# Optimization experiments

Hardware: AMD Instinct MI355X
Metric: run time of the kernel (lower is better)

The kernel has to match this reference:

```python
import jax, jax.numpy as jnp
import numpy as np

B, LAT, MEM, IMG = 8192, 256, 200, 128
THRESHOLD = 1.0 / MEM          # sparse-addressing threshold 1/MEM_DIM
EPS_SHRINK = 1e-12             # module epsilon
EPS_COS = 1e-8                 # torch CosineSimilarity default eps
EPS_L1 = 1e-12                 # torch F.normalize default eps


def setup_inputs() -> dict:
    key = jax.random.key(0)
    k1, k2, k3 = jax.random.split(key, 3)
    z = jax.random.normal(k1, (B, LAT), dtype=jnp.float32)          # encoder latent
    memory = jax.random.normal(k2, (MEM, LAT), dtype=jnp.float32) * 0.05  # kaiming-scale memory
    W = jax.random.normal(k3, (IMG * IMG, LAT), dtype=jnp.float32) * 0.02  # linear weight
    b = jnp.zeros((IMG * IMG,), dtype=jnp.float32)
    return {"z": z, "memory": memory, "W": W, "b": b}


def reference(z, memory, W, b):
    # Cosine similarity via normalized matmul (no [B,MEM,LAT] repeat tensors)
    zn = jnp.linalg.norm(z, axis=1, keepdims=True)          # [B,1]
    mn = jnp.linalg.norm(memory, axis=1, keepdims=True)     # [MEM,1]
    logits = (z @ memory.T) / jnp.maximum(zn * mn.T, EPS_COS)  # [B,MEM]
    w = jax.nn.softmax(logits, axis=1)
    # sparse shrinkage: relu(w-t)*w/(|w-t|+eps)
    w = jax.nn.relu(w - THRESHOLD) * w / (jnp.abs(w - THRESHOLD) + EPS_SHRINK)
    # L1 normalize over memory dim
    w = w / jnp.maximum(jnp.sum(jnp.abs(w), axis=1, keepdims=True), EPS_L1)
    z_hat = w @ memory                                      # [B,LAT]
    x_hat = (z_hat @ W.T + b).reshape(-1, 1, IMG, IMG)      # [B,1,128,128]
    return x_hat, z_hat, w
```

## Files before the change

### kernel.cpp

```cpp
#include <hip/hip_runtime.h>
#include <hip/hip_bf16.h>
#include <stdint.h>

#define B_DIM   8192
#define LAT     256
#define MEM_DIM 200
#define MEM_PAD 208
#define NPIX    16384
#define RPB     16
#define CHUNK   25

typedef short bf16x8 __attribute__((ext_vector_type(8)));
typedef float f32x4  __attribute__((ext_vector_type(4)));

__device__ __forceinline__ float wred_sum(float v) {
#pragma unroll
  for (int m = 32; m; m >>= 1) v += __shfl_xor(v, m, 64);
  return v;
}
__device__ __forceinline__ float wred_max(float v) {
#pragma unroll
  for (int m = 32; m; m >>= 1) v = fmaxf(v, __shfl_xor(v, m, 64));
  return v;
}
__device__ __forceinline__ unsigned short f2bf(float f) {
  unsigned u = __builtin_bit_cast(unsigned, f);
  u = u + 0x7FFFu + ((u >> 16) & 1u);
  return (unsigned short)(u >> 16);
}
__device__ __forceinline__ float bf2f(unsigned short h) {
  return __builtin_bit_cast(float, (unsigned)h << 16);
}
__device__ __forceinline__ void split3(float v, unsigned short& h, unsigned short& m,
                                       unsigned short& l) {
  h = f2bf(v);
  float r1 = v - bf2f(h);
  m = f2bf(r1);
  float r2 = r1 - bf2f(m);
  l = f2bf(r2);
}

__global__ void __launch_bounds__(64) mem_norm_kernel(const float* __restrict__ mem,
                                                      float* __restrict__ mn,
                                                      unsigned short* __restrict__ mem_h,
                                                      unsigned short* __restrict__ mem_m,
                                                      unsigned short* __restrict__ mem_l) {
  const int m = blockIdx.x, lane = threadIdx.x;
  if (m >= MEM_DIM) {
    ushort4 zz = {0, 0, 0, 0};
    ((ushort4*)(mem_h + (size_t)m * LAT))[lane] = zz;
    ((ushort4*)(mem_m + (size_t)m * LAT))[lane] = zz;
    ((ushort4*)(mem_l + (size_t)m * LAT))[lane] = zz;
    return;
  }
  float4 v = ((const float4*)(mem + (size_t)m * LAT))[lane];
  ushort4 h, md, l;
  split3(v.x, h.x, md.x, l.x); split3(v.y, h.y, md.y, l.y);
  split3(v.z, h.z, md.z, l.z); split3(v.w, h.w, md.w, l.w);
  ((ushort4*)(mem_h + (size_t)m * LAT))[lane] = h;
  ((ushort4*)(mem_m + (size_t)m * LAT))[lane] = md;
  ((ushort4*)(mem_l + (size_t)m * LAT))[lane] = l;
  float ss = v.x * v.x + v.y * v.y + v.z * v.z + v.w * v.w;
  ss = wred_sum(ss);
  if (lane == 0) mn[m] = sqrtf(ss);
}

__global__ void __launch_bounds__(256) zsplit_kernel(const float* __restrict__ z,
                                                     unsigned short* __restrict__ z_h,
                                                     unsigned short* __restrict__ z_m,
                                                     unsigned short* __restrict__ z_l) {
  const int i = blockIdx.x * 256 + threadIdx.x;
  float4 v = ((const float4*)z)[i];
  ushort4 h, md, l;
  split3(v.x, h.x, md.x, l.x); split3(v.y, h.y, md.y, l.y);
  split3(v.z, h.z, md.z, l.z); split3(v.w, h.w, md.w, l.w);
  ((ushort4*)z_h)[i] = h;
  ((ushort4*)z_m)[i] = md;
  ((ushort4*)z_l)[i] = l;
}

__global__ void __launch_bounds__(256) convert_w_kernel(const float* __restrict__ W,
                                                        unsigned short* __restrict__ Wb) {
  const int i = blockIdx.x * 256 + threadIdx.x;
  float4 v = ((const float4*)W)[i];
  ushort4 o;
  o.x = f2bf(v.x); o.y = f2bf(v.y); o.z = f2bf(v.z); o.w = f2bf(v.w);
  ((ushort4*)Wb)[i] = o;
}

__global__ void __launch_bounds__(256) row_kernel(
    const float* __restrict__ z, const float* __restrict__ mem,
    const float* __restrict__ mn_g,
    const unsigned short* __restrict__ z_h, const unsigned short* __restrict__ z_m,
    const unsigned short* __restrict__ z_l,
    const unsigned short* __restrict__ mem_h, const unsigned short* __restrict__ mem_m,
    const unsigned short* __restrict__ mem_l,
    float* __restrict__ zhat_out, float* __restrict__ w_out,
    unsigned short* __restrict__ zhat_bf) {
  __shared__ float msh[CHUNK * LAT];
  __shared__ float lw[RPB][MEM_DIM];
  __shared__ float mnsh[MEM_DIM];

  const int tid = threadIdx.x;
  const int lane = tid & 63;
  const int wid = tid >> 6;
  const int row0 = blockIdx.x * RPB;

  if (tid < MEM_DIM) mnsh[tid] = mn_g[tid];

  float4 zr[4];
  float zn[4];
#pragma unroll
  for (int r = 0; r < 4; ++r) {
    const int row = row0 + wid * 4 + r;
    zr[r] = *(const float4*)(z + (size_t)row * LAT + lane * 4);
    float ss = zr[r].x * zr[r].x + zr[r].y * zr[r].y + zr[r].z * zr[r].z + zr[r].w * zr[r].w;
    zn[r] = sqrtf(wred_sum(ss));
  }

  {
    const int fr_ = lane & 15;
    const int kq8 = (lane >> 4) * 8;
    const size_t zoff = (size_t)(row0 + fr_) * LAT + kq8;
    const unsigned short* zh_p = z_h + zoff;
    const unsigned short* zm_p = z_m + zoff;
    const unsigned short* zl_p = z_l + zoff;
    for (int nf = wid; nf <= 12; nf += 4) {
      const size_t moff = (size_t)(nf * 16 + fr_) * LAT + kq8;
      const unsigned short* mh_p = mem_h + moff;
      const unsigned short* mm_p = mem_m + moff;
      const unsigned short* ml_p = mem_l + moff;
      f32x4 a = {};
#pragma unroll
      for (int kk = 0; kk < 8; ++kk) {
        bf16x8 zh = *(const bf16x8*)(zh_p + kk * 32);
        bf16x8 zm = *(const bf16x8*)(zm_p + kk * 32);
        bf16x8 zl = *(const bf16x8*)(zl_p + kk * 32);
        bf16x8 mh = *(const bf16x8*)(mh_p + kk * 32);
        bf16x8 mm = *(const bf16x8*)(mm_p + kk * 32);
        bf16x8 ml = *(const bf16x8*)(ml_p + kk * 32);
        a = __builtin_amdgcn_mfma_f32_16x16x32_bf16(zm, mm, a, 0, 0, 0);
        a = __builtin_amdgcn_mfma_f32_16x16x32_bf16(zh, ml, a, 0, 0, 0);
        a = __builtin_amdgcn_mfma_f32_16x16x32_bf16(zl, mh, a, 0, 0, 0);
        a = __builtin_amdgcn_mfma_f32_16x16x32_bf16(zm, mh, a, 0, 0, 0);
        a = __builtin_amdgcn_mfma_f32_16x16x32_bf16(zh, mm, a, 0, 0, 0);
        a = __builtin_amdgcn_mfma_f32_16x16x32_bf16(zh, mh, a, 0, 0, 0);
      }
      const int m = nf * 16 + fr_;
      if (m < MEM_DIM) {
#pragma unroll
        for (int q = 0; q < 4; ++q)
          lw[(lane >> 4) * 4 + q][m] = a[q];
      }
    }
  }
  __syncthreads();

  const float t = 0.005f;
#pragma unroll
  for (int r = 0; r < 4; ++r) {
    const int lr = wid * 4 + r;
    float lg[4];
#pragma unroll
    for (int i = 0; i < 4; ++i) {
      const int m = lane + 64 * i;
      lg[i] = (m < MEM_DIM) ? lw[lr][m] / fmaxf(zn[r] * mnsh[m], 1e-8f) : -1e30f;
    }
    float mx = wred_max(fmaxf(fmaxf(lg[0], lg[1]), fmaxf(lg[2], lg[3])));
    float e[4]; float s = 0.f;
#pragma unroll
    for (int i = 0; i < 4; ++i) {
      const int m = lane + 64 * i;
      e[i] = (m < MEM_DIM) ? expf(lg[i] - mx) : 0.f;
      s += e[i];
    }
    s = wred_sum(s);
    float sv[4]; float l1 = 0.f;
#pragma unroll
    for (int i = 0; i < 4; ++i) {
      const float wv = e[i] / s;
      const float d = wv - t;
      sv[i] = fmaxf(d, 0.f) * wv / (fabsf(d) + 1e-12f);
      l1 += sv[i];
    }
    l1 = wred_sum(l1);
    const float dnm = fmaxf(l1, 1e-12f);
#pragma unroll
    for (int i = 0; i < 4; ++i) {
      const int m = lane + 64 * i;
      if (m < MEM_DIM) {
        const float wn = sv[i] / dnm;
        lw[lr][m] = wn;
        w_out[(size_t)(row0 + lr) * MEM_DIM + m] = wn;
      }
    }
  }

  f32x4 acc[4] = {};
  for (int c = 0; c < 8; ++c) {
    __syncthreads();
    const float4* gsrc = (const float4*)(mem + (size_t)c * CHUNK * LAT);
    float4* msh4 = (float4*)msh;
    for (int i = tid; i < CHUNK * 64; i += 256) msh4[i] = gsrc[i];
    __syncthreads();
    for (int mm = 0; mm < CHUNK; ++mm) {
      float4 mv = ((float4*)msh)[mm * 64 + lane];
      const int m = c * CHUNK + mm;
#pragma unroll
      for (int r = 0; r < 4; ++r) {
        const float wm = lw[wid * 4 + r][m];
        acc[r][0] += wm * mv.x; acc[r][1] += wm * mv.y;
        acc[r][2] += wm * mv.z; acc[r][3] += wm * mv.w;
      }
    }
  }
#pragma unroll
  for (int r = 0; r < 4; ++r) {
    const int row = row0 + wid * 4 + r;
    float4 o; o.x = acc[r][0]; o.y = acc[r][1]; o.z = acc[r][2]; o.w = acc[r][3];
    *(float4*)(zhat_out + (size_t)row * LAT + lane * 4) = o;
    ushort4 ob; ob.x = f2bf(o.x); ob.y = f2bf(o.y); ob.z = f2bf(o.z); ob.w = f2bf(o.w);
    *(ushort4*)(zhat_bf + (size_t)row * LAT + lane * 4) = ob;
  }
}

#define TSTRIDE 68
__global__ void __launch_bounds__(256, 3) gemm_xhat_kernel(
    const unsigned short* __restrict__ A,
    const unsigned short* __restrict__ Bw,
    const float* __restrict__ bias,
    float* __restrict__ C) {
  __shared__ __align__(16) unsigned char smem[49152];

  const int tid = threadIdx.x;
  const int lane = tid & 63;
  const int wid = tid >> 6;

  const int swz = (blockIdx.x & 7) * 1024 + (blockIdx.x >> 3);
  const int st = swz >> 8;
  const int loc = swz & 255;
  const int tm = (st >> 3) * 16 + (loc & 15);
  const int tn = (st & 7) * 16 + (loc >> 4);
  const int brow = tm * 128;
  const int bcol = tn * 128;

  const int wr = wid >> 1, wc = wid & 1;

  const int ch0 = wid * 2;
  const int r0 = ch0 * 16 + (lane >> 2);
  const int kq = (lane & 3) * 8;

  f32x4 acc[4][4] = {};

#define STAGE(bufbase, t)                                                      \
  {                                                                            \
    const int k0_ = (t) * 32;                                                  \
    _Pragma("unroll")                                                          \
    for (int cc = 0; cc < 2; ++cc) {                                           \
      const int r_ = r0 + cc * 16;                                             \
      __builtin_amdgcn_global_load_lds(                                        \
          (const __attribute__((address_space(1))) void*)(const void*)         \
              (A + (size_t)(brow + r_) * LAT + k0_ + kq),                      \
          (__attribute__((address_space(3))) void*)(void*)                     \
              &smem[(bufbase) + (ch0 + cc) * 1024], 16, 0, 0);                 \
      __builtin_amdgcn_global_load_lds(                                        \
          (const __attribute__((address_space(1))) void*)(const void*)         \
              (Bw + (size_t)(bcol + r_) * LAT + k0_ + kq),                     \
          (__attribute__((address_space(3))) void*)(void*)                     \
              &smem[(bufbase) + 8192 + (ch0 + cc) * 1024], 16, 0, 0);          \
    }                                                                          \
  }

  STAGE(0, 0);
  STAGE(16384, 1);
  STAGE(32768, 2);

#pragma unroll
  for (int t = 0; t < 8; ++t) {
    if (t < 6)       asm volatile("s_waitcnt vmcnt(8)" ::: "memory");
    else if (t == 6) asm volatile("s_waitcnt vmcnt(4)" ::: "memory");
    else             asm volatile("s_waitcnt vmcnt(0)" ::: "memory");
    __builtin_amdgcn_sched_barrier(0);
    __builtin_amdgcn_s_barrier();

    const int bufb = (t % 3) * 16384;
    bf16x8 af[4], bfr[4];
#pragma unroll
    for (int mf = 0; mf < 4; ++mf)
      af[mf] = *(const bf16x8*)&smem[bufb + (wr * 64 + mf * 16 + (lane & 15)) * 64 + (lane >> 4) * 16];
#pragma unroll
    for (int nf = 0; nf < 4; ++nf)
      bfr[nf] = *(const bf16x8*)&smem[bufb + 8192 + (wc * 64 + nf * 16 + (lane & 15)) * 64 + (lane >> 4) * 16];

    asm volatile("s_waitcnt lgkmcnt(0)" ::: "memory");
    __builtin_amdgcn_sched_barrier(0);
    __builtin_amdgcn_s_barrier();

    if (t + 3 < 8) STAGE(((t + 3) % 3) * 16384, t + 3);

#pragma unroll
    for (int mf = 0; mf < 4; ++mf)
#pragma unroll
      for (int nf = 0; nf < 4; ++nf)
        acc[mf][nf] = __builtin_amdgcn_mfma_f32_16x16x32_bf16(af[mf], bfr[nf], acc[mf][nf], 0, 0, 0);
  }
#undef STAGE

  __syncthreads();
  float* tt = (float*)(smem + wid * (16 * TSTRIDE * 4));

  const int colq = (lane & 15) * 4;
  const int col0 = bcol + wc * 64 + colq;
  const float4 bv4 = *(const float4*)(bias + col0);

#pragma unroll
  for (int mf = 0; mf < 4; ++mf) {
#pragma unroll
    for (int nf = 0; nf < 4; ++nf) {
      const int cl = nf * 16 + (lane & 15);
#pragma unroll
      for (int q = 0; q < 4; ++q)
        tt[((lane >> 4) * 4 + q) * TSTRIDE + cl] = acc[mf][nf][q];
    }
#pragma unroll
    for (int rr = 0; rr < 4; ++rr) {
      const int rl = rr * 4 + (lane >> 4);
      float4 v = *(const float4*)&tt[rl * TSTRIDE + colq];
      v.x += bv4.x; v.y += bv4.y; v.z += bv4.z; v.w += bv4.w;
      const int row = brow + wr * 64 + mf * 16 + rl;
      *(float4*)&C[(size_t)row * NPIX + col0] = v;
    }
  }
}

extern "C" void kernel_launch(void* const* d_in, const int* in_sizes, int n_in,
                              void* d_out, int out_size, void* d_ws, size_t ws_size,
                              hipStream_t stream) {
  const float* z    = (const float*)d_in[0];
  const float* mem  = (const float*)d_in[1];
  const float* W    = (const float*)d_in[2];
  const float* bias = (const float*)d_in[3];

  float* xhat = (float*)d_out;
  float* zhat = xhat + (size_t)B_DIM * NPIX;
  float* wout = zhat + (size_t)B_DIM * LAT;

  unsigned short* z_h   = (unsigned short*)xhat;
  unsigned short* z_m   = z_h + (size_t)B_DIM * LAT;
  unsigned short* z_l   = z_m + (size_t)B_DIM * LAT;
  unsigned short* mem_h = z_l + (size_t)B_DIM * LAT;
  unsigned short* mem_m = mem_h + (size_t)MEM_PAD * LAT;
  unsigned short* mem_l = mem_m + (size_t)MEM_PAD * LAT;

  unsigned short* Wb  = (unsigned short*)d_ws;
  unsigned short* zhb = Wb + (size_t)NPIX * LAT;
  float* mn = (float*)(zhb + (size_t)B_DIM * LAT);

  mem_norm_kernel<<<MEM_PAD, 64, 0, stream>>>(mem, mn, mem_h, mem_m, mem_l);
  zsplit_kernel<<<(B_DIM * LAT / 4) / 256, 256, 0, stream>>>(z, z_h, z_m, z_l);
  convert_w_kernel<<<(NPIX * LAT / 4) / 256, 256, 0, stream>>>(W, Wb);
  row_kernel<<<B_DIM / RPB, 256, 0, stream>>>(z, mem, mn, z_h, z_m, z_l,
                                              mem_h, mem_m, mem_l, zhat, wout, zhb);
  gemm_xhat_kernel<<<8192, 256, 0, stream>>>(zhb, Wb, bias, xhat);
}
```

Measured before the change: 223.4 us.

## Use double-buffered pipeline and direct MFMA-transposed epilogue in xhat GEMM

Replaces the triple-buffered global_load_lds pipeline with explicit vmcnt waits by a simpler double buffer synchronized with __syncthreads, cutting LDS use to 32KB and raising launch bounds to 4 blocks per CU. It swaps the MFMA operand order so each lane's accumulator holds 4 consecutive columns. That lets the epilogue write float4 directly to C instead of transposing through LDS. The cost is less prefetch depth and a full barrier each iteration, traded for higher occupancy and no LDS round trip in the output store.

```diff
diff --git a/kernel.cpp b/kernel.cpp
--- a/kernel.cpp
+++ b/kernel.cpp
@@ -224,13 +224,10 @@
   }
 }
 
-#define TSTRIDE 68
-__global__ void __launch_bounds__(256, 3) gemm_xhat_kernel(
-    const unsigned short* __restrict__ A,
-    const unsigned short* __restrict__ Bw,
-    const float* __restrict__ bias,
-    float* __restrict__ C) {
-  __shared__ __align__(16) unsigned char smem[49152];
+__global__ void __launch_bounds__(256, 4) gemm_xhat_kernel(
+    const unsigned short* __restrict__ A, const unsigned short* __restrict__ Bw,
+    const float* __restrict__ bias, float* __restrict__ C) {
+  __shared__ __align__(16) unsigned char smem[32768];
 
   const int tid = threadIdx.x;
   const int lane = tid & 63;
@@ -272,18 +269,13 @@
   }
 
   STAGE(0, 0);
-  STAGE(16384, 1);
-  STAGE(32768, 2);
+  __syncthreads();
 
 #pragma unroll
   for (int t = 0; t < 8; ++t) {
-    if (t < 6)       asm volatile("s_waitcnt vmcnt(8)" ::: "memory");
-    else if (t == 6) asm volatile("s_waitcnt vmcnt(4)" ::: "memory");
-    else             asm volatile("s_waitcnt vmcnt(0)" ::: "memory");
-    __builtin_amdgcn_sched_barrier(0);
-    __builtin_amdgcn_s_barrier();
-
-    const int bufb = (t % 3) * 16384;
+    const int bufb = (t & 1) * 16384;
+    if (t < 7) STAGE(bufb ^ 16384, t + 1);
+
     bf16x8 af[4], bfr[4];
 #pragma unroll
     for (int mf = 0; mf < 4; ++mf)
@@ -292,43 +284,31 @@
     for (int nf = 0; nf < 4; ++nf)
       bfr[nf] = *(const bf16x8*)&smem[bufb + 8192 + (wc * 64 + nf * 16 + (lane & 15)) * 64 + (lane >> 4) * 16];
 
-    asm volatile("s_waitcnt lgkmcnt(0)" ::: "memory");
-    __builtin_amdgcn_sched_barrier(0);
-    __builtin_amdgcn_s_barrier();
-
-    if (t + 3 < 8) STAGE(((t + 3) % 3) * 16384, t + 3);
-
 #pragma unroll
     for (int mf = 0; mf < 4; ++mf)
 #pragma unroll
       for (int nf = 0; nf < 4; ++nf)
-        acc[mf][nf] = __builtin_amdgcn_mfma_f32_16x16x32_bf16(af[mf], bfr[nf], acc[mf][nf], 0, 0, 0);
+        acc[mf][nf] = __builtin_amdgcn_mfma_f32_16x16x32_bf16(bfr[nf], af[mf], acc[mf][nf], 0, 0, 0);
+
+    if (t < 7) __syncthreads();
   }
 #undef STAGE
 
-  __syncthreads();
-  float* tt = (float*)(smem + wid * (16 * TSTRIDE * 4));
-
-  const int colq = (lane & 15) * 4;
-  const int col0 = bcol + wc * 64 + colq;
-  const float4 bv4 = *(const float4*)(bias + col0);
+  const int crow0 = brow + wr * 64 + (lane & 15);
+  const int ccol0 = bcol + wc * 64 + (lane >> 4) * 4;
+  float4 bv[4];
+#pragma unroll
+  for (int nf = 0; nf < 4; ++nf)
+    bv[nf] = *(const float4*)(bias + ccol0 + nf * 16);
 
 #pragma unroll
   for (int mf = 0; mf < 4; ++mf) {
+    float* crow_p = C + (size_t)(crow0 + mf * 16) * NPIX;
 #pragma unroll
     for (int nf = 0; nf < 4; ++nf) {
-      const int cl = nf * 16 + (lane & 15);
-#pragma unroll
-      for (int q = 0; q < 4; ++q)
-        tt[((lane >> 4) * 4 + q) * TSTRIDE + cl] = acc[mf][nf][q];
-    }
-#pragma unroll
-    for (int rr = 0; rr < 4; ++rr) {
-      const int rl = rr * 4 + (lane >> 4);
-      float4 v = *(const float4*)&tt[rl * TSTRIDE + colq];
-      v.x += bv4.x; v.y += bv4.y; v.z += bv4.z; v.w += bv4.w;
-      const int row = brow + wr * 64 + mf * 16 + rl;
-      *(float4*)&C[(size_t)row * NPIX + col0] = v;
+      f32x4 v = acc[mf][nf];
+      v[0] += bv[nf].x; v[1] += bv[nf].y; v[2] += bv[nf].z; v[3] += bv[nf].w;
+      *(f32x4*)(crow_p + ccol0 + nf * 16) = v;
     }
   }
 }
```

After: 272.8 us. +22.1%, slower.
